# Kernel optimization log

Measured on AMD Instinct MI355X. Metric: run time of the kernel, lower is better.

The kernel has to match this reference:

```python
import jax, jax.numpy as jnp
import numpy as np

N = 100000
E = 1600000
IN_C, HID_C, OUT_C = 128, 64, 64


def gcn_conv(x, W, b, src, dst, n_nodes):
    """PyG GCNConv: symmetric-normalized aggregation with self loops.
    out = D^{-1/2} (A + I) D^{-1/2} (x W) + b
    Self-loop contribution handled analytically instead of appending edges.
    """
    h = x @ W  # [N, out_c] transform first (smaller message dim)
    # degree including self loop
    deg = jnp.zeros((n_nodes,), dtype=x.dtype).at[dst].add(1.0) + 1.0
    dinv = jax.lax.rsqrt(deg)  # deg >= 1 due to self loops
    norm = dinv[src] * dinv[dst]  # [E]
    msg = h[src] * norm[:, None]  # [E, out_c] gather + scale
    agg = jnp.zeros_like(h).at[dst].add(msg)  # scatter-add
    agg = agg + h * (dinv * dinv)[:, None]  # self-loop term
    return agg + b


def setup_inputs() -> dict:
    key = jax.random.key(0)
    ks = jax.random.split(key, 8)
    x = jax.random.normal(ks[0], (N, IN_C), dtype=jnp.float32)
    edge_index = jax.random.randint(ks[1], (2, E), 0, N, dtype=jnp.int64)
    # Glorot-ish init scale for weights
    W1 = jax.random.normal(ks[2], (IN_C, HID_C), dtype=jnp.float32) * (1.0 / np.sqrt(IN_C))
    b1 = jnp.zeros((HID_C,), dtype=jnp.float32)
    W2 = jax.random.normal(ks[3], (HID_C, OUT_C), dtype=jnp.float32) * (1.0 / np.sqrt(HID_C))
    b2 = jnp.zeros((OUT_C,), dtype=jnp.float32)
    Wd = jax.random.normal(ks[4], (OUT_C, IN_C), dtype=jnp.float32) * (1.0 / np.sqrt(OUT_C))
    bd = jnp.zeros((IN_C,), dtype=jnp.float32)
    return {"x": x, "edge_index": edge_index, "W1": W1, "b1": b1,
            "W2": W2, "b2": b2, "Wd": Wd, "bd": bd}


def reference(x, edge_index, W1, b1, W2, b2, Wd, bd):
    src, dst = edge_index[0], edge_index[1]
    h = jax.nn.relu(gcn_conv(x, W1, b1, src, dst, N))
    z = gcn_conv(h, W2, b2, src, dst, N)
    x_hat = z @ Wd + bd  # dense decoder
    return x_hat
```

## Files before the change

kernel.cpp:

```cpp
#include <hip/hip_runtime.h>

constexpr int N_NODES = 100000;
constexpr int E_EDGES = 1600000;
constexpr int IN_C = 128, HID_C = 64, OUT_C = 64;
constexpr int IN_CP = 132;
constexpr int NPAD = 100096;
constexpr int DUMMY = N_NODES;
constexpr int BKT_SHIFT = 9;
constexpr int BKT_NODES = 512;
constexpr int NBKT = 196;
constexpr int CSR_CAP = 16384;
constexpr int CAPB = 16384;

__device__ __forceinline__ unsigned short f2bf(float f) {
    unsigned int u = __float_as_uint(f);
    unsigned int r = (u + 0x7FFFu + ((u >> 16) & 1u)) >> 16;
    return (unsigned short)r;
}
__device__ __forceinline__ float bflo(unsigned int u) {
    return __uint_as_float(u << 16);
}
__device__ __forceinline__ float bfhi(unsigned int u) {
    return __uint_as_float(u & 0xFFFF0000u);
}

__global__ void p0_zero(int* __restrict__ bcount,
                        unsigned short* __restrict__ g1, unsigned short* __restrict__ g2) {
    int t = threadIdx.x;
    if (t < NBKT) bcount[t] = 0;
    unsigned int* r1 = (unsigned int*)(g1 + (size_t)N_NODES * 64);
    unsigned int* r2 = (unsigned int*)(g2 + (size_t)N_NODES * 64);
    if (t < 64) { r1[t] = 0u; r2[t] = 0u; }
}

__global__ __launch_bounds__(256) void p1c_bin(const int* __restrict__ src,
                                               const int* __restrict__ dst,
                                               int* __restrict__ bcount,
                                               unsigned int* __restrict__ bbuf, int E) {
    __shared__ int lc[NBKT], lbase[NBKT];
    for (int i = threadIdx.x; i < NBKT; i += 256) lc[i] = 0;
    __syncthreads();
    int base = blockIdx.x * 4096;
    int s[16], d[16];
    for (int k = 0; k < 16; ++k) {
        int i = base + k * 256 + threadIdx.x;
        s[k] = (i < E) ? src[i] : -1;
        d[k] = (i < E) ? dst[i] : -1;
        if (d[k] >= 0) atomicAdd(&lc[d[k] >> BKT_SHIFT], 1);
    }
    __syncthreads();
    for (int i = threadIdx.x; i < NBKT; i += 256) {
        int c = lc[i];
        lbase[i] = c ? (i * CAPB + atomicAdd(&bcount[i], c)) : 0;
        lc[i] = 0;
    }
    __syncthreads();
    for (int k = 0; k < 16; ++k) {
        if (d[k] >= 0) {
            int b = d[k] >> BKT_SHIFT;
            int pos = lbase[b] + atomicAdd(&lc[b], 1);
            bbuf[pos] = (unsigned)s[k] | ((unsigned)(d[k] & (BKT_NODES - 1)) << 17);
        }
    }
}

__global__ __launch_bounds__(256) void p2_build(const unsigned int* __restrict__ bbuf,
                                                const int* __restrict__ bcount,
                                                int* __restrict__ csr,
                                                int* __restrict__ rowbeg,
                                                int* __restrict__ rowend,
                                                float* __restrict__ dinv) {
    __shared__ int cnt[BKT_NODES];
    __shared__ int beg[BKT_NODES];
    __shared__ int cur[BKT_NODES];
    __shared__ int tsum[256];
    int b = blockIdx.x;
    int t = threadIdx.x;
    int e0 = b * CAPB, ec = bcount[b];
    cnt[t] = 0; cnt[t + 256] = 0;
    __syncthreads();
    for (int i = t; i < ec; i += 256) {
        unsigned e = bbuf[e0 + i];
        atomicAdd(&cnt[e >> 17], 1);
    }
    __syncthreads();
    int c0 = cnt[2 * t], c1 = cnt[2 * t + 1];
    int a0 = (c0 + 7) & ~7;
    int a1 = (c1 + 7) & ~7;
    tsum[t] = a0 + a1;
    __syncthreads();
    for (int off = 1; off < 256; off <<= 1) {
        int v = (t >= off) ? tsum[t - off] : 0;
        __syncthreads();
        tsum[t] += v;
        __syncthreads();
    }
    int excl = tsum[t] - (a0 + a1);
    int gb = b * CSR_CAP;
    beg[2 * t] = excl;
    beg[2 * t + 1] = excl + a0;
    cur[2 * t] = 0; cur[2 * t + 1] = 0;
    int n0 = b * BKT_NODES + 2 * t;
    if (n0 < N_NODES) {
        rowbeg[n0] = gb + excl; rowend[n0] = gb + excl + a0;
        dinv[n0] = rsqrtf((float)c0 + 1.0f);
    }
    if (n0 + 1 < N_NODES) {
        rowbeg[n0 + 1] = gb + excl + a0; rowend[n0 + 1] = gb + excl + a0 + a1;
        dinv[n0 + 1] = rsqrtf((float)c1 + 1.0f);
    }
    __syncthreads();
    for (int i = t; i < ec; i += 256) {
        unsigned e = bbuf[e0 + i];
        int ln = e >> 17;
        int pos = beg[ln] + atomicAdd(&cur[ln], 1);
        csr[gb + pos] = (int)(e & 0x1FFFFu);
    }
    __syncthreads();
    {
        int p0 = beg[2 * t] + c0, p0e = beg[2 * t] + a0;
        for (int p = p0; p < p0e; ++p) csr[gb + p] = DUMMY;
        int p1 = beg[2 * t + 1] + c1, p1e = beg[2 * t + 1] + a1;
        for (int p = p1; p < p1e; ++p) csr[gb + p] = DUMMY;
    }
}

__device__ __forceinline__ void gather4(const unsigned short* __restrict__ g,
                                        const int* __restrict__ csr,
                                        int S, int e0, int e1, int e2, int e3, int lane,
                                        float2& A0, float2& A1, float2& A2, float2& A3) {
    const unsigned int* g32 = (const unsigned int*)g;
    int half = lane >> 5;
    int cp = lane & 31;
    float2 a0 = {0.f, 0.f}, a1 = {0.f, 0.f}, a2 = {0.f, 0.f}, a3 = {0.f, 0.f};
    for (int base = S; base < e3; base += 64) {
        int m = min(64, e3 - base);
        int sv = (lane < m) ? csr[base + lane] : 0;
        for (int j = 0; j < m; j += 8) {
            int p = base + j;
            int s0 = __shfl(sv, j + 0 + half);
            int s1 = __shfl(sv, j + 2 + half);
            int s2 = __shfl(sv, j + 4 + half);
            int s3 = __shfl(sv, j + 6 + half);
            unsigned u0 = g32[(size_t)s0 * 32 + cp];
            unsigned u1 = g32[(size_t)s1 * 32 + cp];
            unsigned u2 = g32[(size_t)s2 * 32 + cp];
            unsigned u3 = g32[(size_t)s3 * 32 + cp];
            float tx = (bflo(u0) + bflo(u1)) + (bflo(u2) + bflo(u3));
            float ty = (bfhi(u0) + bfhi(u1)) + (bfhi(u2) + bfhi(u3));
            if (p < e1) {
                if (p < e0) { a0.x += tx; a0.y += ty; } else { a1.x += tx; a1.y += ty; }
            } else {
                if (p < e2) { a2.x += tx; a2.y += ty; } else { a3.x += tx; a3.y += ty; }
            }
        }
    }
    a0.x += __shfl_xor(a0.x, 32); a0.y += __shfl_xor(a0.y, 32);
    a1.x += __shfl_xor(a1.x, 32); a1.y += __shfl_xor(a1.y, 32);
    a2.x += __shfl_xor(a2.x, 32); a2.y += __shfl_xor(a2.y, 32);
    a3.x += __shfl_xor(a3.x, 32); a3.y += __shfl_xor(a3.y, 32);
    A0 = a0; A1 = a1; A2 = a2; A3 = a3;
}

#define ROWOP(ACC, XR)                                                              \
    ACC[0] += XR.x * w0.x + XR.y * w1.x + XR.z * w2.x + XR.w * w3.x;                \
    ACC[1] += XR.x * w0.y + XR.y * w1.y + XR.z * w2.y + XR.w * w3.y;                \
    ACC[2] += XR.x * w0.z + XR.y * w1.z + XR.z * w2.z + XR.w * w3.z;                \
    ACC[3] += XR.x * w0.w + XR.y * w1.w + XR.z * w2.w + XR.w * w3.w;

__global__ __launch_bounds__(256) void gemm1_kernel(const float* __restrict__ x,
                                                    const float* __restrict__ W1,
                                                    const float* __restrict__ dinv,
                                                    unsigned short* __restrict__ g1) {
    __shared__ float xs[64][IN_CP];
    int n0 = blockIdx.x * 64;
    const float4* xv = (const float4*)(x + (size_t)n0 * IN_C);
    int maxv = (min(64, N_NODES - n0)) * (IN_C / 4);
    for (int i = threadIdx.x; i < 64 * (IN_C / 4); i += 256) {
        float4 v = (i < maxv) ? xv[i] : make_float4(0.f, 0.f, 0.f, 0.f);
        *(float4*)&xs[i >> 5][(i & 31) * 4] = v;
    }
    __syncthreads();
    int cg = (threadIdx.x & 15) * 4;
    int ng = (threadIdx.x >> 4) * 4;
    float acc0[4] = {0.f, 0.f, 0.f, 0.f};
    float acc1[4] = {0.f, 0.f, 0.f, 0.f};
    float acc2[4] = {0.f, 0.f, 0.f, 0.f};
    float acc3[4] = {0.f, 0.f, 0.f, 0.f};
#pragma unroll 4
    for (int k = 0; k < IN_C; k += 4) {
        float4 xr0 = *(const float4*)&xs[ng + 0][k];
        float4 xr1 = *(const float4*)&xs[ng + 1][k];
        float4 xr2 = *(const float4*)&xs[ng + 2][k];
        float4 xr3 = *(const float4*)&xs[ng + 3][k];
        float4 w0 = *(const float4*)&W1[(k + 0) * 64 + cg];
        float4 w1 = *(const float4*)&W1[(k + 1) * 64 + cg];
        float4 w2 = *(const float4*)&W1[(k + 2) * 64 + cg];
        float4 w3 = *(const float4*)&W1[(k + 3) * 64 + cg];
        ROWOP(acc0, xr0)
        ROWOP(acc1, xr1)
        ROWOP(acc2, xr2)
        ROWOP(acc3, xr3)
    }
#pragma unroll
    for (int i = 0; i < 4; ++i) {
        int n = n0 + ng + i;
        if (n < N_NODES) {
            float dv = dinv[n];
            const float* a = (i == 0) ? acc0 : (i == 1) ? acc1 : (i == 2) ? acc2 : acc3;
            ushort4 o;
            o.x = f2bf(a[0] * dv);
            o.y = f2bf(a[1] * dv);
            o.z = f2bf(a[2] * dv);
            o.w = f2bf(a[3] * dv);
            *(ushort4*)&g1[(size_t)n * 64 + cg] = o;
        }
    }
}

__global__ __launch_bounds__(256) void fused1_kernel(const unsigned short* __restrict__ g1,
                                                     const int* __restrict__ csr,
                                                     const int* __restrict__ rowbeg,
                                                     const int* __restrict__ rowend,
                                                     const float* __restrict__ dinv,
                                                     const float* __restrict__ b1,
                                                     const float* __restrict__ W2,
                                                     unsigned short* __restrict__ g2) {
    __shared__ float zs[16][64];
    int lane = threadIdx.x & 63;
    int w = threadIdx.x >> 6;
    int cp = lane & 31;
    int d0 = blockIdx.x * 16 + w * 4;
    int S  = __builtin_amdgcn_readfirstlane(rowbeg[d0]);
    int e0 = __builtin_amdgcn_readfirstlane(rowend[d0 + 0]);
    int e1 = __builtin_amdgcn_readfirstlane(rowend[d0 + 1]);
    int e2 = __builtin_amdgcn_readfirstlane(rowend[d0 + 2]);
    int e3 = __builtin_amdgcn_readfirstlane(rowend[d0 + 3]);
    float dv0 = dinv[d0 + 0], dv1 = dinv[d0 + 1], dv2 = dinv[d0 + 2], dv3 = dinv[d0 + 3];
    float2 a0, a1, a2, a3;
    gather4(g1, csr, S, e0, e1, e2, e3, lane, a0, a1, a2, a3);
    const unsigned int* g32 = (const unsigned int*)g1;
    unsigned su0 = g32[(size_t)(d0 + 0) * 32 + cp];
    unsigned su1 = g32[(size_t)(d0 + 1) * 32 + cp];
    unsigned su2 = g32[(size_t)(d0 + 2) * 32 + cp];
    unsigned su3 = g32[(size_t)(d0 + 3) * 32 + cp];
    float2 b1v = *(const float2*)&b1[2 * cp];
    int w4 = w * 4;
    if (lane < 32) {
        float2 z0 = make_float2(fmaxf(dv0 * (a0.x + bflo(su0)) + b1v.x, 0.f),
                                fmaxf(dv0 * (a0.y + bfhi(su0)) + b1v.y, 0.f));
        float2 z1 = make_float2(fmaxf(dv1 * (a1.x + bflo(su1)) + b1v.x, 0.f),
                                fmaxf(dv1 * (a1.y + bfhi(su1)) + b1v.y, 0.f));
        float2 z2 = make_float2(fmaxf(dv2 * (a2.x + bflo(su2)) + b1v.x, 0.f),
                                fmaxf(dv2 * (a2.y + bfhi(su2)) + b1v.y, 0.f));
        float2 z3 = make_float2(fmaxf(dv3 * (a3.x + bflo(su3)) + b1v.x, 0.f),
                                fmaxf(dv3 * (a3.y + bfhi(su3)) + b1v.y, 0.f));
        *(float2*)&zs[w4 + 0][2 * cp] = z0;
        *(float2*)&zs[w4 + 1][2 * cp] = z1;
        *(float2*)&zs[w4 + 2][2 * cp] = z2;
        *(float2*)&zs[w4 + 3][2 * cp] = z3;
    }
    float c0 = 0.f, c1 = 0.f, c2 = 0.f, c3 = 0.f;
#pragma unroll 8
    for (int k = 0; k < HID_C; ++k) {
        float wv = W2[k * 64 + lane];
        c0 += zs[w4 + 0][k] * wv;
        c1 += zs[w4 + 1][k] * wv;
        c2 += zs[w4 + 2][k] * wv;
        c3 += zs[w4 + 3][k] * wv;
    }
    g2[(size_t)(d0 + 0) * 64 + lane] = f2bf(dv0 * c0);
    g2[(size_t)(d0 + 1) * 64 + lane] = f2bf(dv1 * c1);
    g2[(size_t)(d0 + 2) * 64 + lane] = f2bf(dv2 * c2);
    g2[(size_t)(d0 + 3) * 64 + lane] = f2bf(dv3 * c3);
}

__global__ __launch_bounds__(256) void fused2_kernel(const unsigned short* __restrict__ g2,
                                                     const int* __restrict__ csr,
                                                     const int* __restrict__ rowbeg,
                                                     const int* __restrict__ rowend,
                                                     const float* __restrict__ dinv,
                                                     const float* __restrict__ b2,
                                                     const float* __restrict__ Wd,
                                                     const float* __restrict__ bd,
                                                     float* __restrict__ out) {
    __shared__ float zs[16][64];
    int lane = threadIdx.x & 63;
    int w = threadIdx.x >> 6;
    int cp = lane & 31;
    int d0 = blockIdx.x * 16 + w * 4;
    int S  = __builtin_amdgcn_readfirstlane(rowbeg[d0]);
    int e0 = __builtin_amdgcn_readfirstlane(rowend[d0 + 0]);
    int e1 = __builtin_amdgcn_readfirstlane(rowend[d0 + 1]);
    int e2 = __builtin_amdgcn_readfirstlane(rowend[d0 + 2]);
    int e3 = __builtin_amdgcn_readfirstlane(rowend[d0 + 3]);
    float dv0 = dinv[d0 + 0], dv1 = dinv[d0 + 1], dv2 = dinv[d0 + 2], dv3 = dinv[d0 + 3];
    float2 a0, a1, a2, a3;
    gather4(g2, csr, S, e0, e1, e2, e3, lane, a0, a1, a2, a3);
    const unsigned int* g32 = (const unsigned int*)g2;
    unsigned su0 = g32[(size_t)(d0 + 0) * 32 + cp];
    unsigned su1 = g32[(size_t)(d0 + 1) * 32 + cp];
    unsigned su2 = g32[(size_t)(d0 + 2) * 32 + cp];
    unsigned su3 = g32[(size_t)(d0 + 3) * 32 + cp];
    float2 b2v = *(const float2*)&b2[2 * cp];
    int w4 = w * 4;
    if (lane < 32) {
        float2 z0 = make_float2(dv0 * (a0.x + bflo(su0)) + b2v.x, dv0 * (a0.y + bfhi(su0)) + b2v.y);
        float2 z1 = make_float2(dv1 * (a1.x + bflo(su1)) + b2v.x, dv1 * (a1.y + bfhi(su1)) + b2v.y);
        float2 z2 = make_float2(dv2 * (a2.x + bflo(su2)) + b2v.x, dv2 * (a2.y + bfhi(su2)) + b2v.y);
        float2 z3 = make_float2(dv3 * (a3.x + bflo(su3)) + b2v.x, dv3 * (a3.y + bfhi(su3)) + b2v.y);
        *(float2*)&zs[w4 + 0][2 * cp] = z0;
        *(float2*)&zs[w4 + 1][2 * cp] = z1;
        *(float2*)&zs[w4 + 2][2 * cp] = z2;
        *(float2*)&zs[w4 + 3][2 * cp] = z3;
    }
    float bdl = bd[lane], bdh = bd[64 + lane];
    float c0l = bdl, c0h = bdh, c1l = bdl, c1h = bdh;
    float c2l = bdl, c2h = bdh, c3l = bdl, c3h = bdh;
#pragma unroll 8
    for (int k = 0; k < OUT_C; ++k) {
        float w0 = Wd[k * 128 + lane];
        float w1 = Wd[k * 128 + 64 + lane];
        float z0 = zs[w4 + 0][k], z1 = zs[w4 + 1][k], z2 = zs[w4 + 2][k], z3 = zs[w4 + 3][k];
        c0l += z0 * w0; c0h += z0 * w1;
        c1l += z1 * w0; c1h += z1 * w1;
        c2l += z2 * w0; c2h += z2 * w1;
        c3l += z3 * w0; c3h += z3 * w1;
    }
    out[(size_t)(d0 + 0) * 128 + lane] = c0l; out[(size_t)(d0 + 0) * 128 + 64 + lane] = c0h;
    out[(size_t)(d0 + 1) * 128 + lane] = c1l; out[(size_t)(d0 + 1) * 128 + 64 + lane] = c1h;
    out[(size_t)(d0 + 2) * 128 + lane] = c2l; out[(size_t)(d0 + 2) * 128 + 64 + lane] = c2h;
    out[(size_t)(d0 + 3) * 128 + lane] = c3l; out[(size_t)(d0 + 3) * 128 + 64 + lane] = c3h;
}

extern "C" void kernel_launch(void* const* d_in, const int* in_sizes, int n_in,
                              void* d_out, int out_size, void* d_ws, size_t ws_size,
                              hipStream_t stream) {
    const float* x = (const float*)d_in[0];
    const int* ei = (const int*)d_in[1];
    const int* src = ei;
    const int* dst = ei + E_EDGES;
    const float* W1 = (const float*)d_in[2];
    const float* b1 = (const float*)d_in[3];
    const float* W2 = (const float*)d_in[4];
    const float* b2 = (const float*)d_in[5];
    const float* Wd = (const float*)d_in[6];
    const float* bd = (const float*)d_in[7];
    float* out = (float*)d_out;

    int* bcount = (int*)d_ws;
    int* rowbeg = bcount + 256;
    int* rowend = rowbeg + NPAD;
    float* dinv = (float*)(rowend + NPAD);
    int* csr = (int*)(dinv + NPAD);
    unsigned short* g2 = (unsigned short*)(csr + NBKT * CSR_CAP);
    unsigned short* g1 = (unsigned short*)out;
    unsigned int* bbuf = (unsigned int*)((char*)d_out + 16000000);

    const int B = 256;
    const int EB = (E_EDGES + 4095) / 4096;

    p0_zero<<<1, B, 0, stream>>>(bcount, g1, g2);
    p1c_bin<<<EB, B, 0, stream>>>(src, dst, bcount, bbuf, E_EDGES);
    p2_build<<<NBKT, B, 0, stream>>>(bbuf, bcount, csr, rowbeg, rowend, dinv);

    gemm1_kernel<<<(N_NODES + 63) / 64, B, 0, stream>>>(x, W1, dinv, g1);
    fused1_kernel<<<N_NODES / 16, B, 0, stream>>>(g1, csr, rowbeg, rowend, dinv, b1, W2, g2);
    fused2_kernel<<<N_NODES / 16, B, 0, stream>>>(g2, csr, rowbeg, rowend, dinv, b2, Wd, bd, out);
}
```

Before: 197.7 us.

## Fold self-loops into CSR and process eight nodes per wavefront

The CSR build now inserts each node's own index as the first entry of its row, so the self-loop term is picked up by the normal gather instead of a separate load and add. The fused aggregation+GEMM kernels now handle eight destination nodes per wavefront (32 per block) with two gather4 calls. They read activations from LDS as float4 and reuse each weight load across eight rows. This reduces weight traffic per node and raises memory-level parallelism, at the cost of more registers and fewer blocks. Padding to multiples of 8 can also grow, since the extra entry pushes some rows into the next padding group.

```diff
diff --git a/kernel.cpp b/kernel.cpp
--- a/kernel.cpp
+++ b/kernel.cpp
@@ -84,7 +84,8 @@
         atomicAdd(&cnt[e >> 17], 1);
     }
     __syncthreads();
-    int c0 = cnt[2 * t], c1 = cnt[2 * t + 1];
+    int c0 = cnt[2 * t] + 1;
+    int c1 = cnt[2 * t + 1] + 1;
     int a0 = (c0 + 7) & ~7;
     int a1 = (c1 + 7) & ~7;
     tsum[t] = a0 + a1;
@@ -99,15 +100,17 @@
     int gb = b * CSR_CAP;
     beg[2 * t] = excl;
     beg[2 * t + 1] = excl + a0;
-    cur[2 * t] = 0; cur[2 * t + 1] = 0;
+    cur[2 * t] = 1; cur[2 * t + 1] = 1;
     int n0 = b * BKT_NODES + 2 * t;
     if (n0 < N_NODES) {
         rowbeg[n0] = gb + excl; rowend[n0] = gb + excl + a0;
-        dinv[n0] = rsqrtf((float)c0 + 1.0f);
+        dinv[n0] = rsqrtf((float)c0);
+        csr[gb + excl] = n0;
     }
     if (n0 + 1 < N_NODES) {
         rowbeg[n0 + 1] = gb + excl + a0; rowend[n0 + 1] = gb + excl + a0 + a1;
-        dinv[n0 + 1] = rsqrtf((float)c1 + 1.0f);
+        dinv[n0 + 1] = rsqrtf((float)c1);
+        csr[gb + excl + a0] = n0 + 1;
     }
     __syncthreads();
     for (int i = t; i < ec; i += 256) {
@@ -226,53 +229,71 @@
                                                      const float* __restrict__ b1,
                                                      const float* __restrict__ W2,
                                                      unsigned short* __restrict__ g2) {
-    __shared__ float zs[16][64];
+    __shared__ float zs[32][64];
     int lane = threadIdx.x & 63;
     int w = threadIdx.x >> 6;
     int cp = lane & 31;
-    int d0 = blockIdx.x * 16 + w * 4;
-    int S  = __builtin_amdgcn_readfirstlane(rowbeg[d0]);
+    int d0 = blockIdx.x * 32 + w * 8;
+    int S0 = __builtin_amdgcn_readfirstlane(rowbeg[d0]);
+    int S1 = __builtin_amdgcn_readfirstlane(rowbeg[d0 + 4]);
     int e0 = __builtin_amdgcn_readfirstlane(rowend[d0 + 0]);
     int e1 = __builtin_amdgcn_readfirstlane(rowend[d0 + 1]);
     int e2 = __builtin_amdgcn_readfirstlane(rowend[d0 + 2]);
     int e3 = __builtin_amdgcn_readfirstlane(rowend[d0 + 3]);
+    int e4 = __builtin_amdgcn_readfirstlane(rowend[d0 + 4]);
+    int e5 = __builtin_amdgcn_readfirstlane(rowend[d0 + 5]);
+    int e6 = __builtin_amdgcn_readfirstlane(rowend[d0 + 6]);
+    int e7 = __builtin_amdgcn_readfirstlane(rowend[d0 + 7]);
     float dv0 = dinv[d0 + 0], dv1 = dinv[d0 + 1], dv2 = dinv[d0 + 2], dv3 = dinv[d0 + 3];
-    float2 a0, a1, a2, a3;
-    gather4(g1, csr, S, e0, e1, e2, e3, lane, a0, a1, a2, a3);
-    const unsigned int* g32 = (const unsigned int*)g1;
-    unsigned su0 = g32[(size_t)(d0 + 0) * 32 + cp];
-    unsigned su1 = g32[(size_t)(d0 + 1) * 32 + cp];
-    unsigned su2 = g32[(size_t)(d0 + 2) * 32 + cp];
-    unsigned su3 = g32[(size_t)(d0 + 3) * 32 + cp];
+    float dv4 = dinv[d0 + 4], dv5 = dinv[d0 + 5], dv6 = dinv[d0 + 6], dv7 = dinv[d0 + 7];
+    float2 a0, a1, a2, a3, a4, a5, a6, a7;
+    gather4(g1, csr, S0, e0, e1, e2, e3, lane, a0, a1, a2, a3);
+    gather4(g1, csr, S1, e4, e5, e6, e7, lane, a4, a5, a6, a7);
     float2 b1v = *(const float2*)&b1[2 * cp];
-    int w4 = w * 4;
+    int w8 = w * 8;
     if (lane < 32) {
-        float2 z0 = make_float2(fmaxf(dv0 * (a0.x + bflo(su0)) + b1v.x, 0.f),
-                                fmaxf(dv0 * (a0.y + bfhi(su0)) + b1v.y, 0.f));
-        float2 z1 = make_float2(fmaxf(dv1 * (a1.x + bflo(su1)) + b1v.x, 0.f),
-                                fmaxf(dv1 * (a1.y + bfhi(su1)) + b1v.y, 0.f));
-        float2 z2 = make_float2(fmaxf(dv2 * (a2.x + bflo(su2)) + b1v.x, 0.f),
-                                fmaxf(dv2 * (a2.y + bfhi(su2)) + b1v.y, 0.f));
-        float2 z3 = make_float2(fmaxf(dv3 * (a3.x + bflo(su3)) + b1v.x, 0.f),
-                                fmaxf(dv3 * (a3.y + bfhi(su3)) + b1v.y, 0.f));
-        *(float2*)&zs[w4 + 0][2 * cp] = z0;
-        *(float2*)&zs[w4 + 1][2 * cp] = z1;
-        *(float2*)&zs[w4 + 2][2 * cp] = z2;
-        *(float2*)&zs[w4 + 3][2 * cp] = z3;
-    }
-    float c0 = 0.f, c1 = 0.f, c2 = 0.f, c3 = 0.f;
-#pragma unroll 8
-    for (int k = 0; k < HID_C; ++k) {
-        float wv = W2[k * 64 + lane];
-        c0 += zs[w4 + 0][k] * wv;
-        c1 += zs[w4 + 1][k] * wv;
-        c2 += zs[w4 + 2][k] * wv;
-        c3 += zs[w4 + 3][k] * wv;
-    }
-    g2[(size_t)(d0 + 0) * 64 + lane] = f2bf(dv0 * c0);
-    g2[(size_t)(d0 + 1) * 64 + lane] = f2bf(dv1 * c1);
-    g2[(size_t)(d0 + 2) * 64 + lane] = f2bf(dv2 * c2);
-    g2[(size_t)(d0 + 3) * 64 + lane] = f2bf(dv3 * c3);
+        *(float2*)&zs[w8 + 0][2 * cp] = make_float2(fmaxf(dv0 * a0.x + b1v.x, 0.f), fmaxf(dv0 * a0.y + b1v.y, 0.f));
+        *(float2*)&zs[w8 + 1][2 * cp] = make_float2(fmaxf(dv1 * a1.x + b1v.x, 0.f), fmaxf(dv1 * a1.y + b1v.y, 0.f));
+        *(float2*)&zs[w8 + 2][2 * cp] = make_float2(fmaxf(dv2 * a2.x + b1v.x, 0.f), fmaxf(dv2 * a2.y + b1v.y, 0.f));
+        *(float2*)&zs[w8 + 3][2 * cp] = make_float2(fmaxf(dv3 * a3.x + b1v.x, 0.f), fmaxf(dv3 * a3.y + b1v.y, 0.f));
+        *(float2*)&zs[w8 + 4][2 * cp] = make_float2(fmaxf(dv4 * a4.x + b1v.x, 0.f), fmaxf(dv4 * a4.y + b1v.y, 0.f));
+        *(float2*)&zs[w8 + 5][2 * cp] = make_float2(fmaxf(dv5 * a5.x + b1v.x, 0.f), fmaxf(dv5 * a5.y + b1v.y, 0.f));
+        *(float2*)&zs[w8 + 6][2 * cp] = make_float2(fmaxf(dv6 * a6.x + b1v.x, 0.f), fmaxf(dv6 * a6.y + b1v.y, 0.f));
+        *(float2*)&zs[w8 + 7][2 * cp] = make_float2(fmaxf(dv7 * a7.x + b1v.x, 0.f), fmaxf(dv7 * a7.y + b1v.y, 0.f));
+    }
+    float c_[8];
+#pragma unroll
+    for (int r = 0; r < 8; ++r) c_[r] = 0.f;
+    for (int k4 = 0; k4 < HID_C; k4 += 4) {
+        float4 z0 = *(const float4*)&zs[w8 + 0][k4];
+        float4 z1 = *(const float4*)&zs[w8 + 1][k4];
+        float4 z2 = *(const float4*)&zs[w8 + 2][k4];
+        float4 z3 = *(const float4*)&zs[w8 + 3][k4];
+        float4 z4 = *(const float4*)&zs[w8 + 4][k4];
+        float4 z5 = *(const float4*)&zs[w8 + 5][k4];
+        float4 z6 = *(const float4*)&zs[w8 + 6][k4];
+        float4 z7 = *(const float4*)&zs[w8 + 7][k4];
+#pragma unroll
+        for (int kk = 0; kk < 4; ++kk) {
+            float wv = W2[(k4 + kk) * 64 + lane];
+            c_[0] += ((const float*)&z0)[kk] * wv;
+            c_[1] += ((const float*)&z1)[kk] * wv;
+            c_[2] += ((const float*)&z2)[kk] * wv;
+            c_[3] += ((const float*)&z3)[kk] * wv;
+            c_[4] += ((const float*)&z4)[kk] * wv;
+            c_[5] += ((const float*)&z5)[kk] * wv;
+            c_[6] += ((const float*)&z6)[kk] * wv;
+            c_[7] += ((const float*)&z7)[kk] * wv;
+        }
+    }
+    g2[(size_t)(d0 + 0) * 64 + lane] = f2bf(dv0 * c_[0]);
+    g2[(size_t)(d0 + 1) * 64 + lane] = f2bf(dv1 * c_[1]);
+    g2[(size_t)(d0 + 2) * 64 + lane] = f2bf(dv2 * c_[2]);
+    g2[(size_t)(d0 + 3) * 64 + lane] = f2bf(dv3 * c_[3]);
+    g2[(size_t)(d0 + 4) * 64 + lane] = f2bf(dv4 * c_[4]);
+    g2[(size_t)(d0 + 5) * 64 + lane] = f2bf(dv5 * c_[5]);
+    g2[(size_t)(d0 + 6) * 64 + lane] = f2bf(dv6 * c_[6]);
+    g2[(size_t)(d0 + 7) * 64 + lane] = f2bf(dv7 * c_[7]);
 }
 
 __global__ __launch_bounds__(256) void fused2_kernel(const unsigned short* __restrict__ g2,
@@ -284,53 +305,71 @@
                                                      const float* __restrict__ Wd,
                                                      const float* __restrict__ bd,
                                                      float* __restrict__ out) {
-    __shared__ float zs[16][64];
+    __shared__ float zs[32][64];
     int lane = threadIdx.x & 63;
     int w = threadIdx.x >> 6;
     int cp = lane & 31;
-    int d0 = blockIdx.x * 16 + w * 4;
-    int S  = __builtin_amdgcn_readfirstlane(rowbeg[d0]);
+    int d0 = blockIdx.x * 32 + w * 8;
+    int S0 = __builtin_amdgcn_readfirstlane(rowbeg[d0]);
+    int S1 = __builtin_amdgcn_readfirstlane(rowbeg[d0 + 4]);
     int e0 = __builtin_amdgcn_readfirstlane(rowend[d0 + 0]);
     int e1 = __builtin_amdgcn_readfirstlane(rowend[d0 + 1]);
     int e2 = __builtin_amdgcn_readfirstlane(rowend[d0 + 2]);
     int e3 = __builtin_amdgcn_readfirstlane(rowend[d0 + 3]);
+    int e4 = __builtin_amdgcn_readfirstlane(rowend[d0 + 4]);
+    int e5 = __builtin_amdgcn_readfirstlane(rowend[d0 + 5]);
+    int e6 = __builtin_amdgcn_readfirstlane(rowend[d0 + 6]);
+    int e7 = __builtin_amdgcn_readfirstlane(rowend[d0 + 7]);
     float dv0 = dinv[d0 + 0], dv1 = dinv[d0 + 1], dv2 = dinv[d0 + 2], dv3 = dinv[d0 + 3];
-    float2 a0, a1, a2, a3;
-    gather4(g2, csr, S, e0, e1, e2, e3, lane, a0, a1, a2, a3);
-    const unsigned int* g32 = (const unsigned int*)g2;
-    unsigned su0 = g32[(size_t)(d0 + 0) * 32 + cp];
-    unsigned su1 = g32[(size_t)(d0 + 1) * 32 + cp];
-    unsigned su2 = g32[(size_t)(d0 + 2) * 32 + cp];
-    unsigned su3 = g32[(size_t)(d0 + 3) * 32 + cp];
+    float dv4 = dinv[d0 + 4], dv5 = dinv[d0 + 5], dv6 = dinv[d0 + 6], dv7 = dinv[d0 + 7];
+    float2 a0, a1, a2, a3, a4, a5, a6, a7;
+    gather4(g2, csr, S0, e0, e1, e2, e3, lane, a0, a1, a2, a3);
+    gather4(g2, csr, S1, e4, e5, e6, e7, lane, a4, a5, a6, a7);
     float2 b2v = *(const float2*)&b2[2 * cp];
-    int w4 = w * 4;
+    int w8 = w * 8;
     if (lane < 32) {
-        float2 z0 = make_float2(dv0 * (a0.x + bflo(su0)) + b2v.x, dv0 * (a0.y + bfhi(su0)) + b2v.y);
-        float2 z1 = make_float2(dv1 * (a1.x + bflo(su1)) + b2v.x, dv1 * (a1.y + bfhi(su1)) + b2v.y);
-        float2 z2 = make_float2(dv2 * (a2.x + bflo(su2)) + b2v.x, dv2 * (a2.y + bfhi(su2)) + b2v.y);
-        float2 z3 = make_float2(dv3 * (a3.x + bflo(su3)) + b2v.x, dv3 * (a3.y + bfhi(su3)) + b2v.y);
-        *(float2*)&zs[w4 + 0][2 * cp] = z0;
-        *(float2*)&zs[w4 + 1][2 * cp] = z1;
-        *(float2*)&zs[w4 + 2][2 * cp] = z2;
-        *(float2*)&zs[w4 + 3][2 * cp] = z3;
+        *(float2*)&zs[w8 + 0][2 * cp] = make_float2(dv0 * a0.x + b2v.x, dv0 * a0.y + b2v.y);
+        *(float2*)&zs[w8 + 1][2 * cp] = make_float2(dv1 * a1.x + b2v.x, dv1 * a1.y + b2v.y);
+        *(float2*)&zs[w8 + 2][2 * cp] = make_float2(dv2 * a2.x + b2v.x, dv2 * a2.y + b2v.y);
+        *(float2*)&zs[w8 + 3][2 * cp] = make_float2(dv3 * a3.x + b2v.x, dv3 * a3.y + b2v.y);
+        *(float2*)&zs[w8 + 4][2 * cp] = make_float2(dv4 * a4.x + b2v.x, dv4 * a4.y + b2v.y);
+        *(float2*)&zs[w8 + 5][2 * cp] = make_float2(dv5 * a5.x + b2v.x, dv5 * a5.y + b2v.y);
+        *(float2*)&zs[w8 + 6][2 * cp] = make_float2(dv6 * a6.x + b2v.x, dv6 * a6.y + b2v.y);
+        *(float2*)&zs[w8 + 7][2 * cp] = make_float2(dv7 * a7.x + b2v.x, dv7 * a7.y + b2v.y);
     }
     float bdl = bd[lane], bdh = bd[64 + lane];
-    float c0l = bdl, c0h = bdh, c1l = bdl, c1h = bdh;
-    float c2l = bdl, c2h = bdh, c3l = bdl, c3h = bdh;
-#pragma unroll 8
-    for (int k = 0; k < OUT_C; ++k) {
-        float w0 = Wd[k * 128 + lane];
-        float w1 = Wd[k * 128 + 64 + lane];
-        float z0 = zs[w4 + 0][k], z1 = zs[w4 + 1][k], z2 = zs[w4 + 2][k], z3 = zs[w4 + 3][k];
-        c0l += z0 * w0; c0h += z0 * w1;
-        c1l += z1 * w0; c1h += z1 * w1;
-        c2l += z2 * w0; c2h += z2 * w1;
-        c3l += z3 * w0; c3h += z3 * w1;
-    }
-    out[(size_t)(d0 + 0) * 128 + lane] = c0l; out[(size_t)(d0 + 0) * 128 + 64 + lane] = c0h;
-    out[(size_t)(d0 + 1) * 128 + lane] = c1l; out[(size_t)(d0 + 1) * 128 + 64 + lane] = c1h;
-    out[(size_t)(d0 + 2) * 128 + lane] = c2l; out[(size_t)(d0 + 2) * 128 + 64 + lane] = c2h;
-    out[(size_t)(d0 + 3) * 128 + lane] = c3l; out[(size_t)(d0 + 3) * 128 + 64 + lane] = c3h;
+    float cl_[8], ch_[8];
+#pragma unroll
+    for (int r = 0; r < 8; ++r) { cl_[r] = bdl; ch_[r] = bdh; }
+    for (int k4 = 0; k4 < OUT_C; k4 += 4) {
+        float4 z0 = *(const float4*)&zs[w8 + 0][k4];
+        float4 z1 = *(const float4*)&zs[w8 + 1][k4];
+        float4 z2 = *(const float4*)&zs[w8 + 2][k4];
+        float4 z3 = *(const float4*)&zs[w8 + 3][k4];
+        float4 z4 = *(const float4*)&zs[w8 + 4][k4];
+        float4 z5 = *(const float4*)&zs[w8 + 5][k4];
+        float4 z6 = *(const float4*)&zs[w8 + 6][k4];
+        float4 z7 = *(const float4*)&zs[w8 + 7][k4];
+#pragma unroll
+        for (int kk = 0; kk < 4; ++kk) {
+            float w0 = Wd[(k4 + kk) * 128 + lane];
+            float w1 = Wd[(k4 + kk) * 128 + 64 + lane];
+            float zz;
+            zz = ((const float*)&z0)[kk]; cl_[0] += zz * w0; ch_[0] += zz * w1;
+            zz = ((const float*)&z1)[kk]; cl_[1] += zz * w0; ch_[1] += zz * w1;
+            zz = ((const float*)&z2)[kk]; cl_[2] += zz * w0; ch_[2] += zz * w1;
+            zz = ((const float*)&z3)[kk]; cl_[3] += zz * w0; ch_[3] += zz * w1;
+            zz = ((const float*)&z4)[kk]; cl_[4] += zz * w0; ch_[4] += zz * w1;
+            zz = ((const float*)&z5)[kk]; cl_[5] += zz * w0; ch_[5] += zz * w1;
+            zz = ((const float*)&z6)[kk]; cl_[6] += zz * w0; ch_[6] += zz * w1;
+            zz = ((const float*)&z7)[kk]; cl_[7] += zz * w0; ch_[7] += zz * w1;
+        }
+    }
+#pragma unroll
+    for (int r = 0; r < 8; ++r) {
+        out[(size_t)(d0 + r) * 128 + lane] = cl_[r];
+        out[(size_t)(d0 + r) * 128 + 64 + lane] = ch_[r];
+    }
 }
 
 extern "C" void kernel_launch(void* const* d_in, const int* in_sizes, int n_in,
@@ -365,6 +404,6 @@
     p2_build<<<NBKT, B, 0, stream>>>(bbuf, bcount, csr, rowbeg, rowend, dinv);
 
     gemm1_kernel<<<(N_NODES + 63) / 64, B, 0, stream>>>(x, W1, dinv, g1);
-    fused1_kernel<<<N_NODES / 16, B, 0, stream>>>(g1, csr, rowbeg, rowend, dinv, b1, W2, g2);
-    fused2_kernel<<<N_NODES / 16, B, 0, stream>>>(g2, csr, rowbeg, rowend, dinv, b2, Wd, bd, out);
-}
+    fused1_kernel<<<N_NODES / 32, B, 0, stream>>>(g1, csr, rowbeg, rowend, dinv, b1, W2, g2);
+    fused2_kernel<<<N_NODES / 32, B, 0, stream>>>(g2, csr, rowbeg, rowend, dinv, b2, Wd, bd, out);
+}
```

After: 215.9 us. +9.2%, slower.
